# Optimization experiments

Measured on AMD Instinct MI355X. Metric: run time of the kernel, lower is better.

Reference implementation:

```python
import jax, jax.numpy as jnp
import numpy as np

N = 100000   # nodes
E = 800000   # edges
D = 64       # hidden_channels
H = 4        # heads
C = D        # out_channels per head (PyG: out_channels=hidden)


def setup_inputs() -> dict:
    key = jax.random.key(0)
    ks = jax.random.split(key, 20)
    inp = {}
    inp['x'] = jax.random.normal(ks[0], (N, D), dtype=jnp.float32)
    inp['edge_index'] = jax.random.randint(ks[1], (2, E), 0, N, dtype=jnp.int32)
    i = 2
    for layer in (1, 2):
        for nm in ('Wq', 'Wk', 'Wv'):
            inp[f'{nm}{layer}'] = jax.random.normal(ks[i], (D, H * C), dtype=jnp.float32) * 0.05; i += 1
            inp[f'b{nm[1]}{layer}'] = jnp.zeros((H * C,), dtype=jnp.float32)
        inp[f'Ws{layer}'] = jax.random.normal(ks[i], (D, D), dtype=jnp.float32) * 0.05; i += 1
        inp[f'bs{layer}'] = jnp.zeros((D,), dtype=jnp.float32)
    return inp


def _transformer_conv(x, src, dst, Wq, bq, Wk, bk, Wv, bv, Ws, bs):
    n = x.shape[0]
    q = (x @ Wq + bq).reshape(n, H, C)
    k = (x @ Wk + bk).reshape(n, H, C)
    v = (x @ Wv + bv).reshape(n, H, C)
    # per-edge attention logits: [E, H]
    alpha = jnp.einsum('ehc,ehc->eh', q[dst], k[src]) / np.sqrt(C).astype(np.float32)
    # segment softmax over incoming edges of each destination node
    amax = jax.ops.segment_max(alpha, dst, num_segments=n)          # [N, H]
    ex = jnp.exp(alpha - amax[dst])                                 # [E, H]
    denom = jax.ops.segment_sum(ex, dst, num_segments=n)           # [N, H]
    attn = ex / (denom[dst] + 1e-16)                                # [E, H]
    msg = v[src] * attn[:, :, None]                                 # [E, H, C]
    agg = jax.ops.segment_sum(msg, dst, num_segments=n)            # [N, H, C]
    # concat=False -> mean over heads; root_weight skip connection
    return agg.mean(axis=1) + x @ Ws + bs


def reference(x, edge_index, Wq1, bq1, Wk1, bk1, Wv1, bv1, Ws1, bs1,
              Wq2, bq2, Wk2, bk2, Wv2, bv2, Ws2, bs2):
    src, dst = edge_index[0], edge_index[1]
    h = _transformer_conv(x, src, dst, Wq1, bq1, Wk1, bk1, Wv1, bv1, Ws1, bs1)
    h = jax.nn.relu(h)
    out = _transformer_conv(h, src, dst, Wq2, bq2, Wk2, bk2, Wv2, bv2, Ws2, bs2)
    return out
```

## Files before the change

### kernel.cpp

```cpp
#include <hip/hip_runtime.h>
#include <hip/hip_fp16.h>
#include <math.h>


typedef __attribute__((ext_vector_type(8))) short bf16x8;
typedef __attribute__((ext_vector_type(4))) float f32x4;
typedef __attribute__((ext_vector_type(2))) float f32x2;

#define QKSCALE 32.0f
#define C_EXP2 1.760325e-4f

__device__ inline unsigned short f2bf(float f) {
    unsigned int u = __float_as_uint(f);
    u = (u + 0x7fffu + ((u >> 16) & 1u)) >> 16;
    return (unsigned short)u;
}

#if __has_builtin(__builtin_amdgcn_cvt_pk_fp8_f32) && __has_builtin(__builtin_amdgcn_cvt_pk_f32_fp8)
#define HW_FP8 1
#endif

#ifndef HW_FP8
__device__ inline unsigned int fp8_enc1(float f) {
    unsigned int u = __float_as_uint(f);
    unsigned int s = (u >> 24) & 0x80u;
    float a = fabsf(f);
    if (a >= 448.f) return s | 0x7Eu;
    if (a < 0.015625f) return s;
    unsigned int ua = __float_as_uint(a);
    unsigned int r = ua + 0x7FFFFu + ((ua >> 20) & 1u);
    int e = (int)((r >> 23) & 255u) - 120;
    unsigned int m = (r >> 20) & 7u;
    if (e < 1) return s;
    if (e > 15) return s | 0x7Eu;
    return s | (unsigned int)((e << 3) | m);
}
__device__ inline float fp8_dec1(unsigned int b) {
    unsigned int e = (b >> 3) & 15u, m = b & 7u;
    float v;
    if (e) v = __uint_as_float(((e + 120u) << 23) | (m << 20));
    else   v = (float)m * 0.001953125f;
    return (b & 0x80u) ? -v : v;
}
#endif

__device__ inline unsigned int fp8x4_pack(float f0, float f1, float f2, float f3) {
#ifdef HW_FP8
    int pk = __builtin_amdgcn_cvt_pk_fp8_f32(f0, f1, 0, false);
    pk = __builtin_amdgcn_cvt_pk_fp8_f32(f2, f3, pk, true);
    return (unsigned int)pk;
#else
    return fp8_enc1(f0) | (fp8_enc1(f1) << 8) | (fp8_enc1(f2) << 16) | (fp8_enc1(f3) << 24);
#endif
}

__device__ inline float4 fp8x4_unpack(unsigned int k) {
#ifdef HW_FP8
    f32x2 lo = __builtin_amdgcn_cvt_pk_f32_fp8((int)k, false);
    f32x2 hi = __builtin_amdgcn_cvt_pk_f32_fp8((int)k, true);
    return make_float4(lo[0], lo[1], hi[0], hi[1]);
#else
    return make_float4(fp8_dec1(k & 255u), fp8_dec1((k >> 8) & 255u),
                       fp8_dec1((k >> 16) & 255u), fp8_dec1(k >> 24));
#endif
}

__device__ inline unsigned int i8x4_pack(float f0, float f1, float f2, float f3) {
    int a = (int)rintf(f0 * QKSCALE); a = a < -127 ? -127 : (a > 127 ? 127 : a);
    int b = (int)rintf(f1 * QKSCALE); b = b < -127 ? -127 : (b > 127 ? 127 : b);
    int c = (int)rintf(f2 * QKSCALE); c = c < -127 ? -127 : (c > 127 ? 127 : c);
    int d = (int)rintf(f3 * QKSCALE); d = d < -127 ? -127 : (d > 127 ? 127 : d);
    return (unsigned int)((a & 255) | ((b & 255) << 8) | ((c & 255) << 16) | ((d & 255) << 24));
}

__device__ inline int sdot4(unsigned int a, unsigned int b, int c) {
#if __has_builtin(__builtin_amdgcn_sdot4)
    return __builtin_amdgcn_sdot4((int)a, (int)b, c, false);
#else
    int r = c;
#pragma unroll
    for (int i = 0; i < 4; ++i) {
        int ai = (int)(a << (24 - 8 * i)) >> 24;
        int bi = (int)(b << (24 - 8 * i)) >> 24;
        r += ai * bi;
    }
    return r;
#endif
}

__global__ void k_setup(
    const float* __restrict__ x, unsigned short* __restrict__ Xb, int ncast4,
    const float* __restrict__ Wq1, const float* __restrict__ Wk1,
    const float* __restrict__ Wv1, const float* __restrict__ Ws1,
    const float* __restrict__ Wq2, const float* __restrict__ Wk2,
    const float* __restrict__ Wv2, const float* __restrict__ Ws2,
    unsigned short* __restrict__ Wt,
    int* __restrict__ counts, int N, int castBl)
{
    int b = blockIdx.x, tid = threadIdx.x;
    if (b < castBl) {
        int i = b * 256 + tid;
        if (i < ncast4) {
            float4 v = ((const float4*)x)[i];
            ushort4 o;
            o.x = f2bf(v.x); o.y = f2bf(v.y); o.z = f2bf(v.z); o.w = f2bf(v.w);
            ((ushort4*)Xb)[i] = o;
        }
    } else if (b < castBl + 416) {
        int j = (b - castBl) * 256 + tid;
        int layer = j / 53248;
        int r = j % 53248;
        if (r < 49152) {
            int m = r / 16384, w = r % 16384;
            int n = w / 64, k = w % 64;
            const float* W = (layer == 0)
                ? ((m == 0) ? Wq1 : (m == 1) ? Wk1 : Wv1)
                : ((m == 0) ? Wq2 : (m == 1) ? Wk2 : Wv2);
            Wt[layer * 53248 + m * 16384 + n * 64 + k] = f2bf(W[k * 256 + n]);
        } else {
            int w = r - 49152;
            int n = w / 64, k = w % 64;
            const float* W = (layer == 0) ? Ws1 : Ws2;
            Wt[layer * 53248 + 49152 + n * 64 + k] = f2bf(W[k * 64 + n]);
        }
    } else {
        int i = (b - castBl - 416) * 256 + tid;
        if (i < N) counts[i] = 0;
    }
}

#define SCAN_B 256
#define SCAN_CHUNK 2048
__global__ void k_scan1(const int* __restrict__ counts, int n,
                        int* __restrict__ offs, int* __restrict__ bsums) {
    __shared__ int lds[SCAN_B];
    int b = blockIdx.x, tid = threadIdx.x;
    int base = b * SCAN_CHUNK + tid * 8;
    int v[8]; int s = 0;
#pragma unroll
    for (int i = 0; i < 8; ++i) { int idx = base + i; int c = (idx < n) ? counts[idx] : 0; v[i] = s; s += c; }
    lds[tid] = s;
    for (int off = 1; off < SCAN_B; off <<= 1) {
        __syncthreads();
        int x = (tid >= off) ? lds[tid - off] : 0;
        __syncthreads();
        lds[tid] += x;
    }
    __syncthreads();
    int texcl = lds[tid] - s;
#pragma unroll
    for (int i = 0; i < 8; ++i) { int idx = base + i; if (idx < n) offs[idx] = texcl + v[i]; }
    if (tid == SCAN_B - 1) bsums[b] = lds[tid];
}

__global__ void k_scan2(int* bsums, int nb) {
    __shared__ int lds[256];
    int t = threadIdx.x;
    if (nb > 256) {
        if (t == 0) { int s = 0; for (int i = 0; i < nb; ++i) { int c = bsums[i]; bsums[i] = s; s += c; } }
        return;
    }
    int v = (t < nb) ? bsums[t] : 0;
    lds[t] = v;
    for (int off = 1; off < 256; off <<= 1) {
        __syncthreads();
        int x = (t >= off) ? lds[t - off] : 0;
        __syncthreads();
        lds[t] += x;
    }
    __syncthreads();
    if (t < nb) bsums[t] = lds[t] - v;
}

__global__ void k_scatter(const int* __restrict__ src, const int* __restrict__ dst, int E,
                          const int* __restrict__ offs, const int* __restrict__ bsums,
                          const int* __restrict__ rank, int* __restrict__ csr_src) {
    int e = blockIdx.x * 256 + threadIdx.x;
    if (e < E) {
        int d = dst[e];
        csr_src[offs[d] + bsums[d >> 11] + rank[e]] = src[e];
    }
}

#define GROW 272
__global__ __launch_bounds__(256, 4) void k_gemm(
    const unsigned short* __restrict__ Xb, int nrows,
    const unsigned short* __restrict__ WtL,
    const float* __restrict__ bqp, const float* __restrict__ bkp,
    const float* __restrict__ bvp, const float* __restrict__ bsp,
    unsigned char* __restrict__ NB,
    const int* __restrict__ dstp, int histE,
    int* __restrict__ counts, int* __restrict__ rank, int gemmBl)
{
    __shared__ unsigned char st[2][64 * GROW];
    int tid = threadIdx.x;
    if (blockIdx.x >= gemmBl) {
        int e = (blockIdx.x - gemmBl) * 256 + tid;
        if (e < histE) rank[e] = atomicAdd(&counts[dstp[e]], 1);
        return;
    }
    int wave = tid >> 6, lane = tid & 63;
    int quad = lane >> 4, n16 = lane & 15;
    int r0 = blockIdx.x * 64;

    bf16x8 a0[4], a1[4];
#pragma unroll
    for (int g = 0; g < 4; ++g) {
        int node = r0 + g * 16 + n16;
        int nodec = (node < nrows) ? node : (nrows - 1);
        a0[g] = *(const bf16x8*)(Xb + (size_t)nodec * 64 + quad * 8);
        a1[g] = *(const bf16x8*)(Xb + (size_t)nodec * 64 + 32 + quad * 8);
    }

    bf16x8 f[8]; float4 cb[4];
    auto loadW = [&](const unsigned short* W, const float* bp) {
#pragma unroll
        for (int c = 0; c < 4; ++c) {
            int roff = ((wave * 4 + c) * 16 + n16) * 64 + quad * 8;
            f[2 * c]     = *(const bf16x8*)(W + roff);
            f[2 * c + 1] = *(const bf16x8*)(W + roff + 32);
            cb[c]        = *(const float4*)(bp + (wave * 4 + c) * 16 + quad * 4);
        }
    };
    auto stage = [&](int buf, bool isInt8) {
#pragma unroll
        for (int c = 0; c < 4; ++c) {
#pragma unroll
            for (int g = 0; g < 4; ++g) {
                f32x4 acc = {0.f, 0.f, 0.f, 0.f};
                acc = __builtin_amdgcn_mfma_f32_16x16x32_bf16(f[2 * c],     a0[g], acc, 0, 0, 0);
                acc = __builtin_amdgcn_mfma_f32_16x16x32_bf16(f[2 * c + 1], a1[g], acc, 0, 0, 0);
                float f0 = acc[0] + cb[c].x, f1 = acc[1] + cb[c].y;
                float f2 = acc[2] + cb[c].z, f3 = acc[3] + cb[c].w;
                unsigned int pk = isInt8 ? i8x4_pack(f0, f1, f2, f3)
                                         : fp8x4_pack(f0, f1, f2, f3);
                *(unsigned int*)(st[buf] + (g * 16 + n16) * GROW + wave * 64 + c * 16 + quad * 4) = pk;
            }
        }
    };
    auto flush = [&](int buf, int matoff) {
#pragma unroll
        for (int it = 0; it < 4; ++it) {
            int nl = wave * 16 + it * 4 + (lane >> 4);
            uint4 v = *(const uint4*)(st[buf] + nl * GROW + (lane & 15) * 16);
            int node = r0 + nl;
            if (node < nrows)
                *(uint4*)(NB + (size_t)node * 1024 + matoff + (lane & 15) * 16) = v;
        }
    };

    const unsigned short* Wq = WtL;
    const unsigned short* Wk = WtL + 16384;
    const unsigned short* Wv = WtL + 32768;
    const unsigned short* Ws = WtL + 49152;

    loadW(Wq, bqp);
    stage(0, true);
    __syncthreads();

    loadW(Wk, bkp);
    flush(0, 0);
    stage(1, true);
    __syncthreads();

    loadW(Wv, bvp);
    flush(1, 256);
    stage(0, false);
    __syncthreads();

    bf16x8 s0, s1; float4 cs;
    {
        int roff = (wave * 16 + n16) * 64 + quad * 8;
        s0 = *(const bf16x8*)(Ws + roff);
        s1 = *(const bf16x8*)(Ws + roff + 32);
        cs = *(const float4*)(bsp + wave * 16 + quad * 4);
    }
    flush(0, 512);
#pragma unroll
    for (int g = 0; g < 4; ++g) {
        f32x4 acc = {0.f, 0.f, 0.f, 0.f};
        acc = __builtin_amdgcn_mfma_f32_16x16x32_bf16(s0, a0[g], acc, 0, 0, 0);
        acc = __builtin_amdgcn_mfma_f32_16x16x32_bf16(s1, a1[g], acc, 0, 0, 0);
        *(float4*)(st[1] + (g * 16 + n16) * GROW + wave * 64 + quad * 16) =
            make_float4(acc[0] + cs.x, acc[1] + cs.y, acc[2] + cs.z, acc[3] + cs.w);
    }
    __syncthreads();
    flush(1, 768);
}

__global__ __launch_bounds__(256) void k_attn(
    const unsigned char* __restrict__ NB,
    const int* __restrict__ offs, const int* __restrict__ bsums,
    const int* __restrict__ csr_src,
    float* __restrict__ out, unsigned short* __restrict__ Xb,
    int n, int Etot, int mode)
{
    int node = blockIdx.x * 4 + (threadIdx.x >> 6);
    if (node >= n) return;
    int lane = threadIdx.x & 63;
    int sl = lane & 31;
    int half = lane >> 5;
    uint2 q8 = *(const uint2*)(NB + (size_t)node * 1024 + sl * 8);
    int beg = offs[node] + bsums[node >> 11];
    int end = (node + 1 < n) ? (offs[node + 1] + bsums[(node + 1) >> 11]) : Etot;
    float l = 0.f;
    float acc[8];
#pragma unroll
    for (int i = 0; i < 8; ++i) acc[i] = 0.f;
    for (int base = beg; base < end; base += 8) {
        int cnt = end - base; if (cnt > 8) cnt = 8;
        int my = (lane < cnt) ? csr_src[base + lane] : 0;
        uint2 kk[4], vv[4];
#pragma unroll
        for (int p = 0; p < 4; ++p) {
            int idx = __shfl(my, 2 * p + half);
            const unsigned char* row = NB + (size_t)idx * 1024 + 256 + sl * 8;
            kk[p] = *(const uint2*)(row);
            vv[p] = *(const uint2*)(row + 256);
        }
#pragma unroll
        for (int p = 0; p < 4; ++p) {
            int d = sdot4(kk[p].x, q8.x, 0);
            d = sdot4(kk[p].y, q8.y, d);
            d += __shfl_xor(d, 1); d += __shfl_xor(d, 2); d += __shfl_xor(d, 4);
            float w = __builtin_exp2f((float)d * C_EXP2);
            w = (2 * p + half < cnt) ? w : 0.f;
            l += w;
            float4 va = fp8x4_unpack(vv[p].x);
            float4 vb = fp8x4_unpack(vv[p].y);
            acc[0] += va.x * w; acc[1] += va.y * w;
            acc[2] += va.z * w; acc[3] += va.w * w;
            acc[4] += vb.x * w; acc[5] += vb.y * w;
            acc[6] += vb.z * w; acc[7] += vb.w * w;
        }
    }
    l += __shfl_xor(l, 32);
#pragma unroll
    for (int i = 0; i < 8; ++i) acc[i] += __shfl_xor(acc[i], 32);
    float inv = 1.f / (l + 1e-16f);
#pragma unroll
    for (int i = 0; i < 8; ++i) acc[i] *= inv;
#pragma unroll
    for (int i = 0; i < 8; ++i) {
        acc[i] += __shfl_xor(acc[i], 8);
        acc[i] += __shfl_xor(acc[i], 16);
        acc[i] *= 0.25f;
    }
    if (lane < 8) {
        const float* Srow = (const float*)(NB + (size_t)node * 1024 + 768);
        float4 s0 = *(const float4*)(Srow + lane * 8);
        float4 s1 = *(const float4*)(Srow + lane * 8 + 4);
        float r0 = acc[0] + s0.x, r1 = acc[1] + s0.y;
        float r2 = acc[2] + s0.z, r3 = acc[3] + s0.w;
        float r4 = acc[4] + s1.x, r5 = acc[5] + s1.y;
        float r6 = acc[6] + s1.z, r7 = acc[7] + s1.w;
        if (mode == 1) {
            r0 = fmaxf(r0, 0.f); r1 = fmaxf(r1, 0.f);
            r2 = fmaxf(r2, 0.f); r3 = fmaxf(r3, 0.f);
            r4 = fmaxf(r4, 0.f); r5 = fmaxf(r5, 0.f);
            r6 = fmaxf(r6, 0.f); r7 = fmaxf(r7, 0.f);
            uint4 o;
            o.x = (unsigned int)f2bf(r0) | ((unsigned int)f2bf(r1) << 16);
            o.y = (unsigned int)f2bf(r2) | ((unsigned int)f2bf(r3) << 16);
            o.z = (unsigned int)f2bf(r4) | ((unsigned int)f2bf(r5) << 16);
            o.w = (unsigned int)f2bf(r6) | ((unsigned int)f2bf(r7) << 16);
            *(uint4*)(Xb + (size_t)node * 64 + lane * 8) = o;
        } else {
            *(float4*)(out + (size_t)node * 64 + lane * 8) = make_float4(r0, r1, r2, r3);
            *(float4*)(out + (size_t)node * 64 + lane * 8 + 4) = make_float4(r4, r5, r6, r7);
        }
    }
}

extern "C" void kernel_launch(void* const* d_in, const int* in_sizes, int n_in,
                              void* d_out, int out_size, void* d_ws, size_t ws_size,
                              hipStream_t stream)
{
    const float* x  = (const float*)d_in[0];
    const int*   ei = (const int*)d_in[1];
    int N = in_sizes[0] / 64;
    int E = in_sizes[1] / 2;
    const int* srcp = ei;
    const int* dstp = ei + E;
    const float* Wq1 = (const float*)d_in[2],  *bq1 = (const float*)d_in[3];
    const float* Wk1 = (const float*)d_in[4],  *bk1 = (const float*)d_in[5];
    const float* Wv1 = (const float*)d_in[6],  *bv1 = (const float*)d_in[7];
    const float* Ws1 = (const float*)d_in[8],  *bs1 = (const float*)d_in[9];
    const float* Wq2 = (const float*)d_in[10], *bq2 = (const float*)d_in[11];
    const float* Wk2 = (const float*)d_in[12], *bk2 = (const float*)d_in[13];
    const float* Wv2 = (const float*)d_in[14], *bv2 = (const float*)d_in[15];
    const float* Ws2 = (const float*)d_in[16], *bs2 = (const float*)d_in[17];
    float* out = (float*)d_out;

    char* ws = (char*)d_ws;
    size_t off = 0;
    auto alloc = [&](size_t bytes) -> void* {
        void* p = ws + off;
        off = (off + bytes + 255) & ~(size_t)255;
        return p;
    };
    unsigned short* Xb = (unsigned short*)alloc((size_t)N * 64 * 2);
    unsigned char* NB  = (unsigned char*)alloc(((size_t)N + 64) * 1024);
    unsigned short* Wt = (unsigned short*)alloc(2 * 53248 * 2);
    int* counts = (int*)alloc((size_t)N * 4);
    int* rank   = (int*)alloc((size_t)E * 4);
    int* offs   = (int*)alloc((size_t)N * 4);
    int* bsums  = (int*)alloc(1024 * 4);
    int* csr    = (int*)alloc((size_t)E * 4);
    (void)n_in; (void)out_size;
    if (off > ws_size) return;

    int ebl = (E + 255) / 256;
    int nb_scan = (N + SCAN_CHUNK - 1) / SCAN_CHUNK;
    int row_bl = (N + 63) / 64;
    int attn_bl = (N + 3) / 4;
    int ncast4 = N * 16;
    int castBl = (ncast4 + 255) / 256;
    int zeroBl = (N + 255) / 256;

    k_setup<<<castBl + 416 + zeroBl, 256, 0, stream>>>(
        x, Xb, ncast4, Wq1, Wk1, Wv1, Ws1, Wq2, Wk2, Wv2, Ws2, Wt, counts, N, castBl);

    k_gemm<<<row_bl + ebl, 256, 0, stream>>>(
        Xb, N, Wt, bq1, bk1, bv1, bs1, NB,
        dstp, E, counts, rank, row_bl);

    k_scan1<<<nb_scan, SCAN_B, 0, stream>>>(counts, N, offs, bsums);
    k_scan2<<<1, 256, 0, stream>>>(bsums, nb_scan);
    k_scatter<<<ebl, 256, 0, stream>>>(srcp, dstp, E, offs, bsums, rank, csr);

    k_attn<<<attn_bl, 256, 0, stream>>>(NB, offs, bsums, csr, out, Xb, N, E, 1);

    k_gemm<<<row_bl, 256, 0, stream>>>(
        Xb, N, Wt + 53248, bq2, bk2, bv2, bs2, NB,
        dstp, 0, counts, rank, row_bl);

    k_attn<<<attn_bl, 256, 0, stream>>>(NB, offs, bsums, csr, out, Xb, N, E, 0);
}
```

Before: 384.6 us.

## Split projection GEMM across two 128-thread blocks with per-wave private staging

```diff
diff --git a/kernel.cpp b/kernel.cpp
--- a/kernel.cpp
+++ b/kernel.cpp
@@ -182,8 +182,8 @@
     }
 }
 
-#define GROW 272
-__global__ __launch_bounds__(256, 4) void k_gemm(
+#define GST 68
+__global__ __launch_bounds__(128, 8) void k_gemm(
     const unsigned short* __restrict__ Xb, int nrows,
     const unsigned short* __restrict__ WtL,
     const float* __restrict__ bqp, const float* __restrict__ bkp,
@@ -192,16 +192,18 @@
     const int* __restrict__ dstp, int histE,
     int* __restrict__ counts, int* __restrict__ rank, int gemmBl)
 {
-    __shared__ unsigned char st[2][64 * GROW];
+    __shared__ unsigned char st[2][64 * GST];
     int tid = threadIdx.x;
     if (blockIdx.x >= gemmBl) {
-        int e = (blockIdx.x - gemmBl) * 256 + tid;
+        int e = (blockIdx.x - gemmBl) * 128 + tid;
         if (e < histE) rank[e] = atomicAdd(&counts[dstp[e]], 1);
         return;
     }
-    int wave = tid >> 6, lane = tid & 63;
+    int wv = tid >> 6, lane = tid & 63;
+    int qtr = ((blockIdx.x & 1) << 1) | wv;
     int quad = lane >> 4, n16 = lane & 15;
-    int r0 = blockIdx.x * 64;
+    int r0 = (blockIdx.x >> 1) * 64;
+    unsigned char* wst = st[wv];
 
     bf16x8 a0[4], a1[4];
 #pragma unroll
@@ -212,40 +214,33 @@
         a1[g] = *(const bf16x8*)(Xb + (size_t)nodec * 64 + 32 + quad * 8);
     }
 
-    bf16x8 f[8]; float4 cb[4];
-    auto loadW = [&](const unsigned short* W, const float* bp) {
+    auto do_mat = [&](const unsigned short* W, const float* bp,
+                      int matoff, bool isInt8) {
 #pragma unroll
         for (int c = 0; c < 4; ++c) {
-            int roff = ((wave * 4 + c) * 16 + n16) * 64 + quad * 8;
-            f[2 * c]     = *(const bf16x8*)(W + roff);
-            f[2 * c + 1] = *(const bf16x8*)(W + roff + 32);
-            cb[c]        = *(const float4*)(bp + (wave * 4 + c) * 16 + quad * 4);
-        }
-    };
-    auto stage = [&](int buf, bool isInt8) {
-#pragma unroll
-        for (int c = 0; c < 4; ++c) {
+            int roff = ((qtr * 4 + c) * 16 + n16) * 64 + quad * 8;
+            bf16x8 w0 = *(const bf16x8*)(W + roff);
+            bf16x8 w1 = *(const bf16x8*)(W + roff + 32);
+            float4 cb = *(const float4*)(bp + (qtr * 4 + c) * 16 + quad * 4);
 #pragma unroll
             for (int g = 0; g < 4; ++g) {
                 f32x4 acc = {0.f, 0.f, 0.f, 0.f};
-                acc = __builtin_amdgcn_mfma_f32_16x16x32_bf16(f[2 * c],     a0[g], acc, 0, 0, 0);
-                acc = __builtin_amdgcn_mfma_f32_16x16x32_bf16(f[2 * c + 1], a1[g], acc, 0, 0, 0);
-                float f0 = acc[0] + cb[c].x, f1 = acc[1] + cb[c].y;
-                float f2 = acc[2] + cb[c].z, f3 = acc[3] + cb[c].w;
+                acc = __builtin_amdgcn_mfma_f32_16x16x32_bf16(w0, a0[g], acc, 0, 0, 0);
+                acc = __builtin_amdgcn_mfma_f32_16x16x32_bf16(w1, a1[g], acc, 0, 0, 0);
+                float f0 = acc[0] + cb.x, f1 = acc[1] + cb.y;
+                float f2 = acc[2] + cb.z, f3 = acc[3] + cb.w;
                 unsigned int pk = isInt8 ? i8x4_pack(f0, f1, f2, f3)
                                          : fp8x4_pack(f0, f1, f2, f3);
-                *(unsigned int*)(st[buf] + (g * 16 + n16) * GROW + wave * 64 + c * 16 + quad * 4) = pk;
+                *(unsigned int*)(wst + (g * 16 + n16) * GST + c * 16 + quad * 4) = pk;
             }
         }
-    };
-    auto flush = [&](int buf, int matoff) {
 #pragma unroll
         for (int it = 0; it < 4; ++it) {
-            int nl = wave * 16 + it * 4 + (lane >> 4);
-            uint4 v = *(const uint4*)(st[buf] + nl * GROW + (lane & 15) * 16);
+            int nl = it * 16 + (lane >> 2);
+            uint4 v = *(const uint4*)(wst + nl * GST + (lane & 3) * 16);
             int node = r0 + nl;
             if (node < nrows)
-                *(uint4*)(NB + (size_t)node * 1024 + matoff + (lane & 15) * 16) = v;
+                *(uint4*)(NB + (size_t)node * 1024 + matoff + qtr * 64 + (lane & 3) * 16) = v;
         }
     };
 
@@ -254,38 +249,26 @@
     const unsigned short* Wv = WtL + 32768;
     const unsigned short* Ws = WtL + 49152;
 
-    loadW(Wq, bqp);
-    stage(0, true);
-    __syncthreads();
-
-    loadW(Wk, bkp);
-    flush(0, 0);
-    stage(1, true);
-    __syncthreads();
-
-    loadW(Wv, bvp);
-    flush(1, 256);
-    stage(0, false);
-    __syncthreads();
-
-    bf16x8 s0, s1; float4 cs;
+    do_mat(Wq, bqp, 0, true);
+    do_mat(Wk, bkp, 256, true);
+    do_mat(Wv, bvp, 512, false);
+
     {
-        int roff = (wave * 16 + n16) * 64 + quad * 8;
-        s0 = *(const bf16x8*)(Ws + roff);
-        s1 = *(const bf16x8*)(Ws + roff + 32);
-        cs = *(const float4*)(bsp + wave * 16 + quad * 4);
-    }
-    flush(0, 512);
-#pragma unroll
-    for (int g = 0; g < 4; ++g) {
-        f32x4 acc = {0.f, 0.f, 0.f, 0.f};
-        acc = __builtin_amdgcn_mfma_f32_16x16x32_bf16(s0, a0[g], acc, 0, 0, 0);
-        acc = __builtin_amdgcn_mfma_f32_16x16x32_bf16(s1, a1[g], acc, 0, 0, 0);
-        *(float4*)(st[1] + (g * 16 + n16) * GROW + wave * 64 + quad * 16) =
-            make_float4(acc[0] + cs.x, acc[1] + cs.y, acc[2] + cs.z, acc[3] + cs.w);
-    }
-    __syncthreads();
-    flush(1, 768);
+        int roff = (qtr * 16 + n16) * 64 + quad * 8;
+        bf16x8 s0 = *(const bf16x8*)(Ws + roff);
+        bf16x8 s1 = *(const bf16x8*)(Ws + roff + 32);
+        float4 cs = *(const float4*)(bsp + qtr * 16 + quad * 4);
+#pragma unroll
+        for (int g = 0; g < 4; ++g) {
+            f32x4 acc = {0.f, 0.f, 0.f, 0.f};
+            acc = __builtin_amdgcn_mfma_f32_16x16x32_bf16(s0, a0[g], acc, 0, 0, 0);
+            acc = __builtin_amdgcn_mfma_f32_16x16x32_bf16(s1, a1[g], acc, 0, 0, 0);
+            int node = r0 + g * 16 + n16;
+            if (node < nrows)
+                *(float4*)(NB + (size_t)node * 1024 + 768 + qtr * 64 + quad * 16) =
+                    make_float4(acc[0] + cs.x, acc[1] + cs.y, acc[2] + cs.z, acc[3] + cs.w);
+        }
+    }
 }
 
 __global__ __launch_bounds__(256) void k_attn(
@@ -413,6 +396,8 @@
     int ebl = (E + 255) / 256;
     int nb_scan = (N + SCAN_CHUNK - 1) / SCAN_CHUNK;
     int row_bl = (N + 63) / 64;
+    int gemm_bl = row_bl * 2;
+    int hist_bl = (E + 127) / 128;
     int attn_bl = (N + 3) / 4;
     int ncast4 = N * 16;
     int castBl = (ncast4 + 255) / 256;
@@ -421,9 +406,9 @@
     k_setup<<<castBl + 416 + zeroBl, 256, 0, stream>>>(
         x, Xb, ncast4, Wq1, Wk1, Wv1, Ws1, Wq2, Wk2, Wv2, Ws2, Wt, counts, N, castBl);
 
-    k_gemm<<<row_bl + ebl, 256, 0, stream>>>(
+    k_gemm<<<gemm_bl + hist_bl, 128, 0, stream>>>(
         Xb, N, Wt, bq1, bk1, bv1, bs1, NB,
-        dstp, E, counts, rank, row_bl);
+        dstp, E, counts, rank, gemm_bl);
 
     k_scan1<<<nb_scan, SCAN_B, 0, stream>>>(counts, N, offs, bsums);
     k_scan2<<<1, 256, 0, stream>>>(bsums, nb_scan);
@@ -431,9 +416,9 @@
 
     k_attn<<<attn_bl, 256, 0, stream>>>(NB, offs, bsums, csr, out, Xb, N, E, 1);
 
-    k_gemm<<<row_bl, 256, 0, stream>>>(
+    k_gemm<<<gemm_bl, 128, 0, stream>>>(
         Xb, N, Wt + 53248, bq2, bk2, bv2, bs2, NB,
-        dstp, 0, counts, rank, row_bl);
+        dstp, 0, counts, rank, gemm_bl);
 
     k_attn<<<attn_bl, 256, 0, stream>>>(NB, offs, bsums, csr, out, Xb, N, E, 0);
 }
```

Result: slower. 533.4 us (+38.7%).
